# Performance work log

Hardware: AMD Instinct MI355X
Metric: run time of the kernel (lower is better)

Reference implementation:

```python
import jax, jax.numpy as jnp
import numpy as np

TOKENS, D_IN = 8192, 1024
E, D_OUT = 8, 1024
H = 2 * D_OUT  # Expert hidden = 2 * num_outputs


def setup_inputs() -> dict:
    key = jax.random.key(0)
    ks = jax.random.split(key, 4)
    s_in = 1.0 / np.sqrt(D_IN)
    s_h = 1.0 / np.sqrt(H)
    return {
        "x": jax.random.normal(ks[0], (TOKENS, D_IN), dtype=jnp.float32),
        "W1": jax.random.normal(ks[1], (E, D_IN, H), dtype=jnp.float32) * s_in,
        "b1": jnp.zeros((E, H), dtype=jnp.float32),
        "W2": jax.random.normal(ks[2], (E, H, D_OUT), dtype=jnp.float32) * s_h,
        "b2": jnp.zeros((E, D_OUT), dtype=jnp.float32),
        "Wg": jax.random.normal(ks[3], (D_IN, E), dtype=jnp.float32) * s_in,
        "bg": jnp.zeros((E,), dtype=jnp.float32),
    }


def reference(x, W1, b1, W2, b2, Wg, bg):
    # Gating: softmax over experts. gates: [N, E]
    gates = jax.nn.softmax(x @ Wg + bg, axis=-1)
    # All experts run densely: batched GEMM over expert axis.
    h = jax.nn.relu(jnp.einsum('nd,edh->neh', x, W1) + b1)       # [N, E, H]
    expert_out = jnp.einsum('neh,ehf->nef', h, W2) + b2          # [N, E, D_OUT]
    # Gate-weighted sum over experts (fused stack*gate->sum).
    return jnp.einsum('nef,ne->nf', expert_out, gates)            # [N, D_OUT]
```

## Files before the change

### kernel.cpp

```cpp
#include <hip/hip_runtime.h>
#include <stdint.h>

#define TOKENS 8192
#define D_IN   1024
#define NEXP   8
#define D_OUT  1024
#define HDIM   2048

typedef __bf16 bf16x8 __attribute__((ext_vector_type(8)));
typedef __bf16 bf16x4 __attribute__((ext_vector_type(4)));
typedef float  f32x4  __attribute__((ext_vector_type(4)));

__device__ __forceinline__ void gload16(const void* g, void* l) {
  __builtin_amdgcn_global_load_lds(
      (const __attribute__((address_space(1))) void*)g,
      (__attribute__((address_space(3))) void*)l,
      16, 0, 0);
}

template <int N>
__device__ __forceinline__ void waitv() {
  if constexpr (N == 0)      asm volatile("s_waitcnt vmcnt(0)" ::: "memory");
  else if constexpr (N == 1) asm volatile("s_waitcnt vmcnt(1)" ::: "memory");
  else if constexpr (N == 2) asm volatile("s_waitcnt vmcnt(2)" ::: "memory");
  else if constexpr (N == 3) asm volatile("s_waitcnt vmcnt(3)" ::: "memory");
  else if constexpr (N == 4) asm volatile("s_waitcnt vmcnt(4)" ::: "memory");
  else if constexpr (N == 5) asm volatile("s_waitcnt vmcnt(5)" ::: "memory");
  else if constexpr (N == 6) asm volatile("s_waitcnt vmcnt(6)" ::: "memory");
  else static_assert(N <= 6, "unsupported vmcnt");
}

__global__ void gate_cvt_kernel(const float* __restrict__ x,
                                const float* __restrict__ Wg,
                                const float* __restrict__ bg,
                                float* __restrict__ gates,
                                __bf16* __restrict__ xb) {
  const int lane = threadIdx.x & 63;
  const int n = blockIdx.x * 4 + (threadIdx.x >> 6);
  float acc[NEXP];
#pragma unroll
  for (int e = 0; e < NEXP; ++e) acc[e] = 0.f;
  const float* xr = x + (size_t)n * D_IN;
  __bf16* xo = xb + (size_t)n * D_IN;
#pragma unroll 4
  for (int d0 = 0; d0 < D_IN; d0 += 64) {
    const int d = d0 + lane;
    float xv = xr[d];
    xo[d] = (__bf16)xv;
    const float* wr = Wg + d * NEXP;
#pragma unroll
    for (int e = 0; e < NEXP; ++e) acc[e] += xv * wr[e];
  }
#pragma unroll
  for (int e = 0; e < NEXP; ++e) {
    float v = acc[e];
#pragma unroll
    for (int off = 32; off > 0; off >>= 1) v += __shfl_down(v, off);
    acc[e] = v;
  }
  if (lane == 0) {
    float mx = -1e30f;
#pragma unroll
    for (int e = 0; e < NEXP; ++e) { acc[e] += bg[e]; mx = fmaxf(mx, acc[e]); }
    float s = 0.f;
#pragma unroll
    for (int e = 0; e < NEXP; ++e) { acc[e] = expf(acc[e] - mx); s += acc[e]; }
    float inv = 1.f / s;
#pragma unroll
    for (int e = 0; e < NEXP; ++e) gates[n * NEXP + e] = acc[e] * inv;
  }
}

__global__ void transpose_cvt_kernel(const float* __restrict__ W,
                                     __bf16* __restrict__ Wt,
                                     int K, int N, int EPG) {
  __shared__ float tile[32][33];
  const int e = blockIdx.z;
  const int ldo = EPG * K;
  const float* Win = W + (size_t)e * K * N;
  __bf16* Wout = Wt + (size_t)(e / EPG) * N * ldo + (size_t)(e % EPG) * K;
  const int n0 = blockIdx.x * 32;
  const int k0 = blockIdx.y * 32;
  const int tx = threadIdx.x & 31;
  const int ty = threadIdx.x >> 5;
#pragma unroll
  for (int r = ty; r < 32; r += 8)
    tile[r][tx] = Win[(size_t)(k0 + r) * N + n0 + tx];
  __syncthreads();
#pragma unroll
  for (int r = ty; r < 32; r += 8)
    Wout[(size_t)(n0 + r) * ldo + k0 + tx] = (__bf16)tile[tx][r];
}

__global__ void merge_kernel(float* __restrict__ out,
                             const float* __restrict__ acc1,
                             const float* __restrict__ gates,
                             const float* __restrict__ b2,
                             int use_acc1) {
  const int idx = blockIdx.x * 256 + threadIdx.x;
  const int n = idx >> 8;
  const int fb = idx & 255;
  float4 o = ((const float4*)out)[idx];
  if (use_acc1) {
    float4 a = ((const float4*)acc1)[idx];
    o.x += a.x; o.y += a.y; o.z += a.z; o.w += a.w;
  }
  const float* g = gates + (size_t)n * NEXP;
#pragma unroll
  for (int e = 0; e < NEXP; ++e) {
    const float ge = g[e];
    float4 b = ((const float4*)(b2 + (size_t)e * D_OUT))[fb];
    o.x += ge * b.x; o.y += ge * b.y; o.z += ge * b.z; o.w += ge * b.w;
  }
  ((float4*)out)[idx] = o;
}

template <int NT, int BM, int BN, int WM, int WN, int EPI>
__global__ __launch_bounds__(NT, 2)
void moe_gemm(const __bf16* __restrict__ A, size_t AZ,
              const __bf16* __restrict__ B, size_t BZ,
              const float* __restrict__ b1g,
              const float* __restrict__ gates,
              int e0,
              __bf16* __restrict__ Hout, size_t HZ, int OCZ, int ldo,
              float* __restrict__ F0, float* __restrict__ F1,
              int first, int M, int N, int K) {
  constexpr int RM = BM / WM, RN = BN / WN;
  constexpr int FM = RM / 16, FN = RN / 16;
  constexpr int HM = FM / 2,  HN = FN / 2;
  constexpr int LA = BM * 4 / NT;
  constexpr int LB = BN * 4 / NT;
  constexpr int AELEM = BM * 64;
  static_assert(HM * HN * 2 == 16, "want 16-MFMA clusters");
  __shared__ alignas(16) __bf16 lds[(BM + BN) * 64];

  const int tid  = threadIdx.x;
  const int lane = tid & 63;
  const int wave = tid >> 6;
  const int wr   = wave / WN;
  const int wc   = wave % WN;
  const int lrow = lane & 15;
  const int khi  = lane >> 4;
  const int sx   = (lrow & 7) << 3;
  const int bz   = blockIdx.z;

  A += (size_t)bz * AZ;
  B += (size_t)bz * BZ;

  const int Gx   = gridDim.x;
  const int nwg  = Gx * gridDim.y;
  const int orig = blockIdx.y * Gx + blockIdx.x;
  const int wgid = (orig & 7) * (nwg >> 3) + (orig >> 3);
  const int bn0  = (wgid % Gx) * BN;
  const int bm0  = (wgid / Gx) * BM;

  const __bf16* srcA[2][LA];
  const __bf16* srcB[2][LB];
#pragma unroll
  for (int q = 0; q < 2; ++q) {
#pragma unroll
    for (int j = 0; j < LA; ++j) {
      int o   = q * (BM * 64) + j * (NT * 16) + tid * 16;
      int row = o >> 7;
      int cb  = (o & 127) ^ ((row & 7) << 4);
      srcA[q][j] = A + (size_t)(bm0 + row) * K + (cb >> 1);
    }
#pragma unroll
    for (int j = 0; j < LB; ++j) {
      int o   = q * (BN * 64) + j * (NT * 16) + tid * 16;
      int row = o >> 7;
      int cb  = (o & 127) ^ ((row & 7) << 4);
      srcB[q][j] = B + (size_t)(bn0 + row) * K + (cb >> 1);
    }
  }

  auto stageA = [&](int kt, int q) {
#pragma unroll
    for (int j = 0; j < LA; ++j)
      gload16(srcA[q][j] + (size_t)kt * 64,
              lds + q * (BM * 32) + j * (NT * 8) + wave * 512);
  };
  auto stageB = [&](int kt, int q) {
#pragma unroll
    for (int j = 0; j < LB; ++j)
      gload16(srcB[q][j] + (size_t)kt * 64,
              lds + AELEM + q * (BN * 32) + j * (NT * 8) + wave * 512);
  };

  f32x4 acc[FM][FN];
#pragma unroll
  for (int m = 0; m < FM; ++m)
#pragma unroll
    for (int n = 0; n < FN; ++n) acc[m][n] = f32x4{0.f, 0.f, 0.f, 0.f};

  bf16x8 af[HM][2];
  bf16x8 bf[2][HN][2];

  auto rdA = [&](int mq) {
#pragma unroll
    for (int mi = 0; mi < HM; ++mi)
#pragma unroll
      for (int kk = 0; kk < 2; ++kk)
        af[mi][kk] = *(const bf16x8*)
            &lds[(size_t)(mq * (BM / 2) + wr * (RM / 2) + mi * 16 + lrow) * 64 +
                 ((kk * 32 + khi * 8) ^ sx)];
  };
  auto rdB = [&](int nq) {
#pragma unroll
    for (int ni = 0; ni < HN; ++ni)
#pragma unroll
      for (int kk = 0; kk < 2; ++kk)
        bf[nq][ni][kk] = *(const bf16x8*)
            &lds[AELEM +
                 (size_t)(nq * (BN / 2) + wc * (RN / 2) + ni * 16 + lrow) * 64 +
                 ((kk * 32 + khi * 8) ^ sx)];
  };
  auto cluster = [&](int mq, int nq) {
    __builtin_amdgcn_s_setprio(1);
#pragma unroll
    for (int kk = 0; kk < 2; ++kk)
#pragma unroll
      for (int mi = 0; mi < HM; ++mi)
#pragma unroll
        for (int ni = 0; ni < HN; ++ni)
          acc[mq * HM + mi][nq * HN + ni] =
              __builtin_amdgcn_mfma_f32_16x16x32_bf16(
                  af[mi][kk], bf[nq][ni][kk], acc[mq * HM + mi][nq * HN + ni],
                  0, 0, 0);
    __builtin_amdgcn_s_setprio(0);
  };

#define BAR()   asm volatile("s_barrier" ::: "memory")
#define LGKM0() do { asm volatile("s_waitcnt lgkmcnt(0)" ::: "memory"); \
                     __builtin_amdgcn_sched_barrier(0); } while (0)

  const int nk = K >> 6;

  stageA(0, 0); stageB(0, 0); stageB(0, 1);
  waitv<LB>();
  BAR();

  for (int t = 0; t < nk; ++t) {
    const bool pf = (t + 1 < nk);

    rdA(0); rdB(0);
    stageA(t, 1);
    BAR(); LGKM0();
    cluster(0, 0);
    waitv<LA>();
    BAR();
    rdB(1);
    if (pf) stageA(t + 1, 0);
    BAR(); LGKM0();
    cluster(0, 1);
    if (pf) waitv<LA>(); else waitv<0>();
    BAR();
    rdA(1);
    if (pf) stageB(t + 1, 0);
    BAR(); LGKM0();
    cluster(1, 0);
    BAR();
    if (pf) stageB(t + 1, 1);
    BAR();
    cluster(1, 1);
    if (pf) waitv<LB>();
    BAR();
  }

#undef BAR
#undef LGKM0

  const float* bias = (EPI == 0) ? b1g + (size_t)(e0 + bz) * HDIM : nullptr;
  const int ecol = e0 + bz;
  __bf16* Hp = (EPI == 0) ? Hout + (size_t)bz * HZ + (size_t)bz * OCZ : nullptr;
  float* F = (EPI == 3) ? (bz ? F1 : F0) : nullptr;

#pragma unroll
  for (int m = 0; m < FM; ++m) {
    const int grow0 = bm0 + (m / HM) * (BM / 2) + wr * (RM / 2) +
                      (m % HM) * 16 + khi * 4;
    if constexpr (EPI == 0) {
      float g[4];
#pragma unroll
      for (int r = 0; r < 4; ++r)
        g[r] = gates[(size_t)(grow0 + r) * NEXP + ecol];
#pragma unroll
      for (int n = 0; n < FN; ++n) {
        const int gcol = bn0 + (n / HN) * (BN / 2) + wc * (RN / 2) +
                         (n % HN) * 16 + lrow;
        const float bv = bias[gcol];
        f32x4 a = acc[m][n];
#pragma unroll
        for (int r = 0; r < 4; ++r) {
          float v = a[r] + bv;
          v = v > 0.f ? v : 0.f;
          Hp[(size_t)(grow0 + r) * ldo + gcol] = (__bf16)(v * g[r]);
        }
      }
    } else {
#pragma unroll
      for (int n = 0; n < FN; ++n) {
        const int gcol = bn0 + (n / HN) * (BN / 2) + wc * (RN / 2) +
                         (n % HN) * 16 + lrow;
        f32x4 a = acc[m][n];
#pragma unroll
        for (int r = 0; r < 4; ++r) {
          float* o = F + (size_t)(grow0 + r) * N + gcol;
          if (first) *o = a[r];
          else       *o += a[r];
        }
      }
    }
  }
}

extern "C" void kernel_launch(void* const* d_in, const int* in_sizes, int n_in,
                              void* d_out, int out_size, void* d_ws, size_t ws_size,
                              hipStream_t stream) {
  const float* x  = (const float*)d_in[0];
  const float* W1 = (const float*)d_in[1];
  const float* b1 = (const float*)d_in[2];
  const float* W2 = (const float*)d_in[3];
  const float* b2 = (const float*)d_in[4];
  const float* Wg = (const float*)d_in[5];
  const float* bg = (const float*)d_in[6];
  float* out = (float*)d_out;

  char* w = (char*)d_ws;
  float* gates = (float*)w;   w += (size_t)TOKENS * NEXP * 4;
  __bf16* xb   = (__bf16*)w;  w += (size_t)TOKENS * D_IN * 2;
  __bf16* w1t  = (__bf16*)w;  w += (size_t)NEXP * HDIM * D_IN * 2;
  __bf16* w2c  = (__bf16*)w;  w += (size_t)NEXP * D_OUT * HDIM * 2;
  const size_t base = (size_t)(w - (char*)d_ws);

  const size_t acc_b = (size_t)TOKENS * D_OUT * 4;
  const size_t h1_b  = (size_t)TOKENS * HDIM * 2;
  const int G = (ws_size >= base + acc_b + 4 * h1_b) ? 4
              : (ws_size >= base + acc_b + 2 * h1_b) ? 2 : 1;

  float* acc1 = nullptr;
  if (G > 1) { acc1 = (float*)w; w += acc_b; }
  __bf16* hbuf = (__bf16*)w;

  const size_t WSLICE = (size_t)HDIM * D_IN;

  gate_cvt_kernel<<<TOKENS / 4, 256, 0, stream>>>(x, Wg, bg, gates, xb);
  transpose_cvt_kernel<<<dim3(HDIM / 32, D_IN / 32, NEXP), 256, 0, stream>>>(
      W1, w1t, D_IN, HDIM, 1);
  transpose_cvt_kernel<<<dim3(D_OUT / 32, HDIM / 32, NEXP), 256, 0, stream>>>(
      W2, w2c, HDIM, D_OUT, (G == 4) ? 2 : 1);

  if (G == 4) {
    for (int d = 0; d < 2; ++d) {
      for (int i2 = 0; i2 < 2; ++i2) {
        const int e0 = 4 * d + 2 * i2;
        moe_gemm<512, 256, 256, 2, 4, 0><<<dim3(8, 32, 2), 512, 0, stream>>>(
            xb, 0, w1t + (size_t)e0 * WSLICE, WSLICE, b1, gates, e0,
            hbuf + (size_t)i2 * TOKENS * 4096, 0, HDIM, 2 * HDIM,
            nullptr, nullptr, 0, TOKENS, HDIM, D_IN);
      }
      moe_gemm<256, 256, 128, 2, 2, 3><<<dim3(8, 32, 2), 256, 0, stream>>>(
          hbuf, (size_t)TOKENS * 4096,
          w2c + (size_t)(2 * d) * D_OUT * 4096, (size_t)D_OUT * 4096,
          nullptr, nullptr, 0, nullptr, 0, 0, 2 * HDIM,
          out, acc1, (d == 0) ? 1 : 0, TOKENS, D_OUT, 2 * HDIM);
    }
  } else if (G == 2) {
    for (int d = 0; d < 4; ++d) {
      const int e0 = 2 * d;
      moe_gemm<512, 256, 256, 2, 4, 0><<<dim3(8, 32, 2), 512, 0, stream>>>(
          xb, 0, w1t + (size_t)e0 * WSLICE, WSLICE, b1, gates, e0,
          hbuf, (size_t)TOKENS * HDIM, 0, HDIM,
          nullptr, nullptr, 0, TOKENS, HDIM, D_IN);
      moe_gemm<256, 256, 128, 2, 2, 3><<<dim3(8, 32, 2), 256, 0, stream>>>(
          hbuf, (size_t)TOKENS * HDIM,
          w2c + (size_t)e0 * D_OUT * HDIM, (size_t)D_OUT * HDIM,
          nullptr, nullptr, 0, nullptr, 0, 0, HDIM,
          out, acc1, (d == 0) ? 1 : 0, TOKENS, D_OUT, HDIM);
    }
  } else {
    for (int e = 0; e < NEXP; ++e) {
      moe_gemm<512, 256, 256, 2, 4, 0><<<dim3(8, 32, 1), 512, 0, stream>>>(
          xb, 0, w1t + (size_t)e * WSLICE, 0, b1, gates, e,
          hbuf, 0, 0, HDIM,
          nullptr, nullptr, 0, TOKENS, HDIM, D_IN);
      moe_gemm<256, 256, 128, 2, 2, 3><<<dim3(8, 32, 1), 256, 0, stream>>>(
          hbuf, 0, w2c + (size_t)e * D_OUT * HDIM, 0,
          nullptr, nullptr, 0, nullptr, 0, 0, HDIM,
          out, nullptr, (e == 0) ? 1 : 0, TOKENS, D_OUT, HDIM);
    }
  }

  merge_kernel<<<TOKENS, 256, 0, stream>>>(out, acc1, gates, b2, (G > 1) ? 1 : 0);
}
```

Measured before the change: 661.3 us.

## Split-K second GEMM with atomic accumulation into pre-initialized output

The second expert GEMM now uses the larger 512-thread 256x256 tile and splits its K dimension in two across grid z. Partial sums go straight into the output with float atomics instead of read-modify-write into two accumulators. A new init kernel writes the gate-weighted b2 bias into the output up front, which removes the acc1 buffer and the final merge pass. The cost is atomic traffic and result order that is no longer deterministic. The EPI value 4 must be handled by the epilogue code not shown here.

```diff
diff --git a/kernel.cpp b/kernel.cpp
--- a/kernel.cpp
+++ b/kernel.cpp
@@ -25,9 +25,7 @@
   else if constexpr (N == 2) asm volatile("s_waitcnt vmcnt(2)" ::: "memory");
   else if constexpr (N == 3) asm volatile("s_waitcnt vmcnt(3)" ::: "memory");
   else if constexpr (N == 4) asm volatile("s_waitcnt vmcnt(4)" ::: "memory");
-  else if constexpr (N == 5) asm volatile("s_waitcnt vmcnt(5)" ::: "memory");
-  else if constexpr (N == 6) asm volatile("s_waitcnt vmcnt(6)" ::: "memory");
-  else static_assert(N <= 6, "unsupported vmcnt");
+  else static_assert(N <= 4, "unsupported vmcnt");
 }
 
 __global__ void gate_cvt_kernel(const float* __restrict__ x,
@@ -92,19 +90,13 @@
     Wout[(size_t)(n0 + r) * ldo + k0 + tx] = (__bf16)tile[tx][r];
 }
 
-__global__ void merge_kernel(float* __restrict__ out,
-                             const float* __restrict__ acc1,
-                             const float* __restrict__ gates,
-                             const float* __restrict__ b2,
-                             int use_acc1) {
+__global__ void init_out_kernel(float* __restrict__ out,
+                                const float* __restrict__ gates,
+                                const float* __restrict__ b2) {
   const int idx = blockIdx.x * 256 + threadIdx.x;
   const int n = idx >> 8;
   const int fb = idx & 255;
-  float4 o = ((const float4*)out)[idx];
-  if (use_acc1) {
-    float4 a = ((const float4*)acc1)[idx];
-    o.x += a.x; o.y += a.y; o.z += a.z; o.w += a.w;
-  }
+  float4 o = {0.f, 0.f, 0.f, 0.f};
   const float* g = gates + (size_t)n * NEXP;
 #pragma unroll
   for (int e = 0; e < NEXP; ++e) {
@@ -119,12 +111,13 @@
 __global__ __launch_bounds__(NT, 2)
 void moe_gemm(const __bf16* __restrict__ A, size_t AZ,
               const __bf16* __restrict__ B, size_t BZ,
+              int NKH, int KHO,
               const float* __restrict__ b1g,
               const float* __restrict__ gates,
               int e0,
               __bf16* __restrict__ Hout, size_t HZ, int OCZ, int ldo,
-              float* __restrict__ F0, float* __restrict__ F1,
-              int first, int M, int N, int K) {
+              float* __restrict__ Fout,
+              int M, int N, int Kext, int LDK) {
   constexpr int RM = BM / WM, RN = BN / WN;
   constexpr int FM = RM / 16, FN = RN / 16;
   constexpr int HM = FM / 2,  HN = FN / 2;
@@ -143,9 +136,11 @@
   const int khi  = lane >> 4;
   const int sx   = (lrow & 7) << 3;
   const int bz   = blockIdx.z;
-
-  A += (size_t)bz * AZ;
-  B += (size_t)bz * BZ;
+  const int slice = bz / NKH;
+  const int kh    = bz % NKH;
+
+  A += (size_t)slice * AZ + (size_t)kh * KHO;
+  B += (size_t)slice * BZ + (size_t)kh * KHO;
 
   const int Gx   = gridDim.x;
   const int nwg  = Gx * gridDim.y;
@@ -163,14 +158,14 @@
       int o   = q * (BM * 64) + j * (NT * 16) + tid * 16;
       int row = o >> 7;
       int cb  = (o & 127) ^ ((row & 7) << 4);
-      srcA[q][j] = A + (size_t)(bm0 + row) * K + (cb >> 1);
+      srcA[q][j] = A + (size_t)(bm0 + row) * LDK + (cb >> 1);
     }
 #pragma unroll
     for (int j = 0; j < LB; ++j) {
       int o   = q * (BN * 64) + j * (NT * 16) + tid * 16;
       int row = o >> 7;
       int cb  = (o & 127) ^ ((row & 7) << 4);
-      srcB[q][j] = B + (size_t)(bn0 + row) * K + (cb >> 1);
+      srcB[q][j] = B + (size_t)(bn0 + row) * LDK + (cb >> 1);
     }
   }
 
@@ -234,7 +229,7 @@
 #define LGKM0() do { asm volatile("s_waitcnt lgkmcnt(0)" ::: "memory"); \
                      __builtin_amdgcn_sched_barrier(0); } while (0)
 
-  const int nk = K >> 6;
+  const int nk = Kext >> 6;
 
   stageA(0, 0); stageB(0, 0); stageB(0, 1);
   waitv<LB>();
@@ -270,10 +265,10 @@
 #undef BAR
 #undef LGKM0
 
-  const float* bias = (EPI == 0) ? b1g + (size_t)(e0 + bz) * HDIM : nullptr;
-  const int ecol = e0 + bz;
-  __bf16* Hp = (EPI == 0) ? Hout + (size_t)bz * HZ + (size_t)bz * OCZ : nullptr;
-  float* F = (EPI == 3) ? (bz ? F1 : F0) : nullptr;
+  const float* bias = (EPI == 0) ? b1g + (size_t)(e0 + slice) * HDIM : nullptr;
+  const int ecol = e0 + slice;
+  __bf16* Hp = (EPI == 0) ? Hout + (size_t)slice * HZ + (size_t)slice * OCZ
+                          : nullptr;
 
 #pragma unroll
   for (int m = 0; m < FM; ++m) {
@@ -304,11 +299,8 @@
                          (n % HN) * 16 + lrow;
         f32x4 a = acc[m][n];
 #pragma unroll
-        for (int r = 0; r < 4; ++r) {
-          float* o = F + (size_t)(grow0 + r) * N + gcol;
-          if (first) *o = a[r];
-          else       *o += a[r];
-        }
+        for (int r = 0; r < 4; ++r)
+          unsafeAtomicAdd(Fout + (size_t)(grow0 + r) * N + gcol, a[r]);
       }
     }
   }
@@ -333,18 +325,15 @@
   __bf16* w2c  = (__bf16*)w;  w += (size_t)NEXP * D_OUT * HDIM * 2;
   const size_t base = (size_t)(w - (char*)d_ws);
 
-  const size_t acc_b = (size_t)TOKENS * D_OUT * 4;
-  const size_t h1_b  = (size_t)TOKENS * HDIM * 2;
-  const int G = (ws_size >= base + acc_b + 4 * h1_b) ? 4
-              : (ws_size >= base + acc_b + 2 * h1_b) ? 2 : 1;
-
-  float* acc1 = nullptr;
-  if (G > 1) { acc1 = (float*)w; w += acc_b; }
+  const size_t h1_b = (size_t)TOKENS * HDIM * 2;
+  const int G = (ws_size >= base + 4 * h1_b) ? 4
+              : (ws_size >= base + 2 * h1_b) ? 2 : 1;
   __bf16* hbuf = (__bf16*)w;
 
   const size_t WSLICE = (size_t)HDIM * D_IN;
 
   gate_cvt_kernel<<<TOKENS / 4, 256, 0, stream>>>(x, Wg, bg, gates, xb);
+  init_out_kernel<<<TOKENS, 256, 0, stream>>>(out, gates, b2);
   transpose_cvt_kernel<<<dim3(HDIM / 32, D_IN / 32, NEXP), 256, 0, stream>>>(
       W1, w1t, D_IN, HDIM, 1);
   transpose_cvt_kernel<<<dim3(D_OUT / 32, HDIM / 32, NEXP), 256, 0, stream>>>(
@@ -355,41 +344,39 @@
       for (int i2 = 0; i2 < 2; ++i2) {
         const int e0 = 4 * d + 2 * i2;
         moe_gemm<512, 256, 256, 2, 4, 0><<<dim3(8, 32, 2), 512, 0, stream>>>(
-            xb, 0, w1t + (size_t)e0 * WSLICE, WSLICE, b1, gates, e0,
+            xb, 0, w1t + (size_t)e0 * WSLICE, WSLICE, 1, 0, b1, gates, e0,
             hbuf + (size_t)i2 * TOKENS * 4096, 0, HDIM, 2 * HDIM,
-            nullptr, nullptr, 0, TOKENS, HDIM, D_IN);
+            nullptr, TOKENS, HDIM, D_IN, D_IN);
       }
-      moe_gemm<256, 256, 128, 2, 2, 3><<<dim3(8, 32, 2), 256, 0, stream>>>(
+      moe_gemm<512, 256, 256, 2, 4, 4><<<dim3(4, 32, 4), 512, 0, stream>>>(
           hbuf, (size_t)TOKENS * 4096,
           w2c + (size_t)(2 * d) * D_OUT * 4096, (size_t)D_OUT * 4096,
-          nullptr, nullptr, 0, nullptr, 0, 0, 2 * HDIM,
-          out, acc1, (d == 0) ? 1 : 0, TOKENS, D_OUT, 2 * HDIM);
+          2, 2048, nullptr, nullptr, 0, nullptr, 0, 0, 0,
+          out, TOKENS, D_OUT, 2048, 4096);
     }
   } else if (G == 2) {
     for (int d = 0; d < 4; ++d) {
       const int e0 = 2 * d;
       moe_gemm<512, 256, 256, 2, 4, 0><<<dim3(8, 32, 2), 512, 0, stream>>>(
-          xb, 0, w1t + (size_t)e0 * WSLICE, WSLICE, b1, gates, e0,
+          xb, 0, w1t + (size_t)e0 * WSLICE, WSLICE, 1, 0, b1, gates, e0,
           hbuf, (size_t)TOKENS * HDIM, 0, HDIM,
-          nullptr, nullptr, 0, TOKENS, HDIM, D_IN);
-      moe_gemm<256, 256, 128, 2, 2, 3><<<dim3(8, 32, 2), 256, 0, stream>>>(
+          nullptr, TOKENS, HDIM, D_IN, D_IN);
+      moe_gemm<512, 256, 256, 2, 4, 4><<<dim3(4, 32, 4), 512, 0, stream>>>(
           hbuf, (size_t)TOKENS * HDIM,
           w2c + (size_t)e0 * D_OUT * HDIM, (size_t)D_OUT * HDIM,
-          nullptr, nullptr, 0, nullptr, 0, 0, HDIM,
-          out, acc1, (d == 0) ? 1 : 0, TOKENS, D_OUT, HDIM);
+          2, 1024, nullptr, nullptr, 0, nullptr, 0, 0, 0,
+          out, TOKENS, D_OUT, 1024, HDIM);
     }
   } else {
     for (int e = 0; e < NEXP; ++e) {
       moe_gemm<512, 256, 256, 2, 4, 0><<<dim3(8, 32, 1), 512, 0, stream>>>(
-          xb, 0, w1t + (size_t)e * WSLICE, 0, b1, gates, e,
+          xb, 0, w1t + (size_t)e * WSLICE, 0, 1, 0, b1, gates, e,
           hbuf, 0, 0, HDIM,
-          nullptr, nullptr, 0, TOKENS, HDIM, D_IN);
-      moe_gemm<256, 256, 128, 2, 2, 3><<<dim3(8, 32, 1), 256, 0, stream>>>(
+          nullptr, TOKENS, HDIM, D_IN, D_IN);
+      moe_gemm<512, 256, 256, 2, 4, 4><<<dim3(4, 32, 2), 512, 0, stream>>>(
           hbuf, 0, w2c + (size_t)e * D_OUT * HDIM, 0,
-          nullptr, nullptr, 0, nullptr, 0, 0, HDIM,
-          out, nullptr, (e == 0) ? 1 : 0, TOKENS, D_OUT, HDIM);
-    }
-  }
-
-  merge_kernel<<<TOKENS, 256, 0, stream>>>(out, acc1, gates, b2, (G > 1) ? 1 : 0);
-}
+          2, 1024, nullptr, nullptr, 0, nullptr, 0, 0, 0,
+          out, TOKENS, D_OUT, 1024, HDIM);
+    }
+  }
+}
```

Measured after the change: 766.9 us. 1.16x slower.

## Double-buffer LDS in second expert GEMM and widen its tile to 256x256

Applied to the files above, without the earlier changes.

Adds a DBUF template parameter so the second (down-projection) GEMM keeps two LDS stages, prefetching the whole next K-tile into the alternate slot while the current one is consumed. That GEMM also moves from a 256x128 tile with 256 threads to a 256x256 tile with 512 threads, halving the grid's x dimension. The aim is to hide global-load latency and raise operand reuse per block. The cost is 128 KB of LDS per block, which limits occupancy to one block per CU and may conflict with the launch_bounds hint of two blocks.

```diff
diff --git a/kernel.cpp b/kernel.cpp
--- a/kernel.cpp
+++ b/kernel.cpp
@@ -115,7 +115,7 @@
   ((float4*)out)[idx] = o;
 }
 
-template <int NT, int BM, int BN, int WM, int WN, int EPI>
+template <int NT, int BM, int BN, int WM, int WN, int EPI, int DBUF>
 __global__ __launch_bounds__(NT, 2)
 void moe_gemm(const __bf16* __restrict__ A, size_t AZ,
               const __bf16* __restrict__ B, size_t BZ,
@@ -131,8 +131,9 @@
   constexpr int LA = BM * 4 / NT;
   constexpr int LB = BN * 4 / NT;
   constexpr int AELEM = BM * 64;
+  constexpr int SLOT  = (BM + BN) * 64;
   static_assert(HM * HN * 2 == 16, "want 16-MFMA clusters");
-  __shared__ alignas(16) __bf16 lds[(BM + BN) * 64];
+  __shared__ alignas(16) __bf16 lds[DBUF * SLOT];
 
   const int tid  = threadIdx.x;
   const int lane = tid & 63;
@@ -174,17 +175,17 @@
     }
   }
 
-  auto stageA = [&](int kt, int q) {
+  auto stageA = [&](int kt, int q, int s) {
 #pragma unroll
     for (int j = 0; j < LA; ++j)
       gload16(srcA[q][j] + (size_t)kt * 64,
-              lds + q * (BM * 32) + j * (NT * 8) + wave * 512);
+              lds + s * SLOT + q * (BM * 32) + j * (NT * 8) + wave * 512);
   };
-  auto stageB = [&](int kt, int q) {
+  auto stageB = [&](int kt, int q, int s) {
 #pragma unroll
     for (int j = 0; j < LB; ++j)
       gload16(srcB[q][j] + (size_t)kt * 64,
-              lds + AELEM + q * (BN * 32) + j * (NT * 8) + wave * 512);
+              lds + s * SLOT + AELEM + q * (BN * 32) + j * (NT * 8) + wave * 512);
   };
 
   f32x4 acc[FM][FN];
@@ -196,24 +197,23 @@
   bf16x8 af[HM][2];
   bf16x8 bf[2][HN][2];
 
-  auto rdA = [&](int mq) {
+  auto rdA = [&](const __bf16* As, int mq) {
 #pragma unroll
     for (int mi = 0; mi < HM; ++mi)
 #pragma unroll
       for (int kk = 0; kk < 2; ++kk)
         af[mi][kk] = *(const bf16x8*)
-            &lds[(size_t)(mq * (BM / 2) + wr * (RM / 2) + mi * 16 + lrow) * 64 +
-                 ((kk * 32 + khi * 8) ^ sx)];
+            &As[(size_t)(mq * (BM / 2) + wr * (RM / 2) + mi * 16 + lrow) * 64 +
+                ((kk * 32 + khi * 8) ^ sx)];
   };
-  auto rdB = [&](int nq) {
+  auto rdB = [&](const __bf16* Bs, int nq) {
 #pragma unroll
     for (int ni = 0; ni < HN; ++ni)
 #pragma unroll
       for (int kk = 0; kk < 2; ++kk)
         bf[nq][ni][kk] = *(const bf16x8*)
-            &lds[AELEM +
-                 (size_t)(nq * (BN / 2) + wc * (RN / 2) + ni * 16 + lrow) * 64 +
-                 ((kk * 32 + khi * 8) ^ sx)];
+            &Bs[(size_t)(nq * (BN / 2) + wc * (RN / 2) + ni * 16 + lrow) * 64 +
+                ((kk * 32 + khi * 8) ^ sx)];
   };
   auto cluster = [&](int mq, int nq) {
     __builtin_amdgcn_s_setprio(1);
@@ -236,35 +236,67 @@
 
   const int nk = K >> 6;
 
-  stageA(0, 0); stageB(0, 0); stageB(0, 1);
-  waitv<LB>();
-  BAR();
-
-  for (int t = 0; t < nk; ++t) {
-    const bool pf = (t + 1 < nk);
-
-    rdA(0); rdB(0);
-    stageA(t, 1);
-    BAR(); LGKM0();
-    cluster(0, 0);
-    waitv<LA>();
+  if constexpr (DBUF == 1) {
+    stageA(0, 0, 0); stageB(0, 0, 0); stageB(0, 1, 0);
+    waitv<LB>();
     BAR();
-    rdB(1);
-    if (pf) stageA(t + 1, 0);
-    BAR(); LGKM0();
-    cluster(0, 1);
-    if (pf) waitv<LA>(); else waitv<0>();
+    for (int t = 0; t < nk; ++t) {
+      const bool pf = (t + 1 < nk);
+      rdA(lds, 0); rdB(lds + AELEM, 0);
+      stageA(t, 1, 0);
+      BAR(); LGKM0();
+      cluster(0, 0);
+      waitv<LA>();
+      BAR();
+      rdB(lds + AELEM, 1);
+      if (pf) stageA(t + 1, 0, 0);
+      BAR(); LGKM0();
+      cluster(0, 1);
+      if (pf) waitv<LA>(); else waitv<0>();
+      BAR();
+      rdA(lds, 1);
+      if (pf) stageB(t + 1, 0, 0);
+      BAR(); LGKM0();
+      cluster(1, 0);
+      BAR();
+      if (pf) stageB(t + 1, 1, 0);
+      BAR();
+      cluster(1, 1);
+      if (pf) waitv<LB>();
+      BAR();
+    }
+  } else {
+    stageA(0, 0, 0); stageB(0, 0, 0); stageB(0, 1, 0); stageA(0, 1, 0);
+    waitv<LA + LB>();
     BAR();
-    rdA(1);
-    if (pf) stageB(t + 1, 0);
-    BAR(); LGKM0();
-    cluster(1, 0);
-    BAR();
-    if (pf) stageB(t + 1, 1);
-    BAR();
-    cluster(1, 1);
-    if (pf) waitv<LB>();
-    BAR();
+    for (int t = 0; t < nk; ++t) {
+      const int s = t & 1;
+      const __bf16* As = lds + s * SLOT;
+      const __bf16* Bs = As + AELEM;
+      const bool pf = (t + 1 < nk);
+      rdA(As, 0); rdB(Bs, 0);
+      if (pf) stageA(t + 1, 0, s ^ 1);
+      BAR(); LGKM0();
+      cluster(0, 0);
+      if (pf) waitv<2 * LA>(); else waitv<LA>();
+      BAR();
+      rdB(Bs, 1);
+      if (pf) stageB(t + 1, 0, s ^ 1);
+      BAR(); LGKM0();
+      cluster(0, 1);
+      if (pf) waitv<LA + LB>(); else waitv<0>();
+      BAR();
+      rdA(As, 1);
+      if (pf) stageB(t + 1, 1, s ^ 1);
+      BAR(); LGKM0();
+      cluster(1, 0);
+      BAR();
+      if (pf) stageA(t + 1, 1, s ^ 1);
+      BAR();
+      cluster(1, 1);
+      if (pf) waitv<LA + LB>();
+      BAR();
+    }
   }
 
 #undef BAR
@@ -354,39 +386,39 @@
     for (int d = 0; d < 2; ++d) {
       for (int i2 = 0; i2 < 2; ++i2) {
         const int e0 = 4 * d + 2 * i2;
-        moe_gemm<512, 256, 256, 2, 4, 0><<<dim3(8, 32, 2), 512, 0, stream>>>(
+        moe_gemm<512, 256, 256, 2, 4, 0, 1><<<dim3(8, 32, 2), 512, 0, stream>>>(
             xb, 0, w1t + (size_t)e0 * WSLICE, WSLICE, b1, gates, e0,
             hbuf + (size_t)i2 * TOKENS * 4096, 0, HDIM, 2 * HDIM,
             nullptr, nullptr, 0, TOKENS, HDIM, D_IN);
       }
-      moe_gemm<256, 256, 128, 2, 2, 3><<<dim3(8, 32, 2), 256, 0, stream>>>(
+      moe_gemm<512, 256, 256, 2, 4, 3, 2><<<dim3(4, 32, 2), 512, 0, stream>>>(
           hbuf, (size_t)TOKENS * 4096,
           w2c + (size_t)(2 * d) * D_OUT * 4096, (size_t)D_OUT * 4096,
-          nullptr, nullptr, 0, nullptr, 0, 0, 2 * HDIM,
+          nullptr, nullptr, 0, nullptr, 0, 0, 0,
           out, acc1, (d == 0) ? 1 : 0, TOKENS, D_OUT, 2 * HDIM);
     }
   } else if (G == 2) {
     for (int d = 0; d < 4; ++d) {
       const int e0 = 2 * d;
-      moe_gemm<512, 256, 256, 2, 4, 0><<<dim3(8, 32, 2), 512, 0, stream>>>(
+      moe_gemm<512, 256, 256, 2, 4, 0, 1><<<dim3(8, 32, 2), 512, 0, stream>>>(
           xb, 0, w1t + (size_t)e0 * WSLICE, WSLICE, b1, gates, e0,
           hbuf, (size_t)TOKENS * HDIM, 0, HDIM,
           nullptr, nullptr, 0, TOKENS, HDIM, D_IN);
-      moe_gemm<256, 256, 128, 2, 2, 3><<<dim3(8, 32, 2), 256, 0, stream>>>(
+      moe_gemm<512, 256, 256, 2, 4, 3, 2><<<dim3(4, 32, 2), 512, 0, stream>>>(
           hbuf, (size_t)TOKENS * HDIM,
           w2c + (size_t)e0 * D_OUT * HDIM, (size_t)D_OUT * HDIM,
-          nullptr, nullptr, 0, nullptr, 0, 0, HDIM,
+          nullptr, nullptr, 0, nullptr, 0, 0, 0,
           out, acc1, (d == 0) ? 1 : 0, TOKENS, D_OUT, HDIM);
     }
   } else {
     for (int e = 0; e < NEXP; ++e) {
-      moe_gemm<512, 256, 256, 2, 4, 0><<<dim3(8, 32, 1), 512, 0, stream>>>(
+      moe_gemm<512, 256, 256, 2, 4, 0, 1><<<dim3(8, 32, 1), 512, 0, stream>>>(
           xb, 0, w1t + (size_t)e * WSLICE, 0, b1, gates, e,
           hbuf, 0, 0, HDIM,
           nullptr, nullptr, 0, TOKENS, HDIM, D_IN);
-      moe_gemm<256, 256, 128, 2, 2, 3><<<dim3(8, 32, 1), 256, 0, stream>>>(
+      moe_gemm<512, 256, 256, 2, 4, 3, 2><<<dim3(4, 32, 1), 512, 0, stream>>>(
           hbuf, 0, w2c + (size_t)e * D_OUT * HDIM, 0,
-          nullptr, nullptr, 0, nullptr, 0, 0, HDIM,
+          nullptr, nullptr, 0, nullptr, 0, 0, 0,
           out, nullptr, (e == 0) ? 1 : 0, TOKENS, D_OUT, HDIM);
     }
   }
```

New measurement: 659.2 us. No clear change (-0.3%).

## Concatenate expert hidden states along K and run single-output second GEMM

Applied to the files above, without the earlier changes.

The first GEMM now writes each expert's hidden activations side by side in one wide row buffer (stride G*HDIM), so the second GEMM becomes a single long-K GEMM per group instead of a batched split into two partial outputs. This drops the separate acc1 accumulator, its workspace and the extra read in the merge kernel, and reduces read-modify-write passes over the output. The second GEMM switches to 128x128 tiles with a higher occupancy hint (3 blocks per CU), which gives more blocks but less reuse per tile.

```diff
diff --git a/kernel.cpp b/kernel.cpp
--- a/kernel.cpp
+++ b/kernel.cpp
@@ -25,9 +25,7 @@
   else if constexpr (N == 2) asm volatile("s_waitcnt vmcnt(2)" ::: "memory");
   else if constexpr (N == 3) asm volatile("s_waitcnt vmcnt(3)" ::: "memory");
   else if constexpr (N == 4) asm volatile("s_waitcnt vmcnt(4)" ::: "memory");
-  else if constexpr (N == 5) asm volatile("s_waitcnt vmcnt(5)" ::: "memory");
-  else if constexpr (N == 6) asm volatile("s_waitcnt vmcnt(6)" ::: "memory");
-  else static_assert(N <= 6, "unsupported vmcnt");
+  else static_assert(N <= 4, "unsupported vmcnt");
 }
 
 __global__ void gate_cvt_kernel(const float* __restrict__ x,
@@ -93,18 +91,12 @@
 }
 
 __global__ void merge_kernel(float* __restrict__ out,
-                             const float* __restrict__ acc1,
                              const float* __restrict__ gates,
-                             const float* __restrict__ b2,
-                             int use_acc1) {
+                             const float* __restrict__ b2) {
   const int idx = blockIdx.x * 256 + threadIdx.x;
   const int n = idx >> 8;
   const int fb = idx & 255;
   float4 o = ((const float4*)out)[idx];
-  if (use_acc1) {
-    float4 a = ((const float4*)acc1)[idx];
-    o.x += a.x; o.y += a.y; o.z += a.z; o.w += a.w;
-  }
   const float* g = gates + (size_t)n * NEXP;
 #pragma unroll
   for (int e = 0; e < NEXP; ++e) {
@@ -115,15 +107,15 @@
   ((float4*)out)[idx] = o;
 }
 
-template <int NT, int BM, int BN, int WM, int WN, int EPI>
-__global__ __launch_bounds__(NT, 2)
+template <int NT, int WPE, int BM, int BN, int WM, int WN, int EPI>
+__global__ __launch_bounds__(NT, WPE)
 void moe_gemm(const __bf16* __restrict__ A, size_t AZ,
               const __bf16* __restrict__ B, size_t BZ,
               const float* __restrict__ b1g,
               const float* __restrict__ gates,
               int e0,
-              __bf16* __restrict__ Hout, size_t HZ, int OCZ, int ldo,
-              float* __restrict__ F0, float* __restrict__ F1,
+              __bf16* __restrict__ Hout, int OCZ, int ldo,
+              float* __restrict__ F0,
               int first, int M, int N, int K) {
   constexpr int RM = BM / WM, RN = BN / WN;
   constexpr int FM = RM / 16, FN = RN / 16;
@@ -131,7 +123,7 @@
   constexpr int LA = BM * 4 / NT;
   constexpr int LB = BN * 4 / NT;
   constexpr int AELEM = BM * 64;
-  static_assert(HM * HN * 2 == 16, "want 16-MFMA clusters");
+  static_assert(HM >= 1 && HN >= 1, "tile too small");
   __shared__ alignas(16) __bf16 lds[(BM + BN) * 64];
 
   const int tid  = threadIdx.x;
@@ -272,8 +264,7 @@
 
   const float* bias = (EPI == 0) ? b1g + (size_t)(e0 + bz) * HDIM : nullptr;
   const int ecol = e0 + bz;
-  __bf16* Hp = (EPI == 0) ? Hout + (size_t)bz * HZ + (size_t)bz * OCZ : nullptr;
-  float* F = (EPI == 3) ? (bz ? F1 : F0) : nullptr;
+  __bf16* Hp = (EPI == 0) ? Hout + (size_t)bz * OCZ : nullptr;
 
 #pragma unroll
   for (int m = 0; m < FM; ++m) {
@@ -305,7 +296,7 @@
         f32x4 a = acc[m][n];
 #pragma unroll
         for (int r = 0; r < 4; ++r) {
-          float* o = F + (size_t)(grow0 + r) * N + gcol;
+          float* o = F0 + (size_t)(grow0 + r) * N + gcol;
           if (first) *o = a[r];
           else       *o += a[r];
         }
@@ -333,63 +324,42 @@
   __bf16* w2c  = (__bf16*)w;  w += (size_t)NEXP * D_OUT * HDIM * 2;
   const size_t base = (size_t)(w - (char*)d_ws);
 
-  const size_t acc_b = (size_t)TOKENS * D_OUT * 4;
-  const size_t h1_b  = (size_t)TOKENS * HDIM * 2;
-  const int G = (ws_size >= base + acc_b + 4 * h1_b) ? 4
-              : (ws_size >= base + acc_b + 2 * h1_b) ? 2 : 1;
-
-  float* acc1 = nullptr;
-  if (G > 1) { acc1 = (float*)w; w += acc_b; }
+  const size_t h1_b = (size_t)TOKENS * HDIM * 2;
+  const int G = (ws_size >= base + 4 * h1_b) ? 4
+              : (ws_size >= base + 2 * h1_b) ? 2 : 1;
   __bf16* hbuf = (__bf16*)w;
 
   const size_t WSLICE = (size_t)HDIM * D_IN;
+  const int KB = G * HDIM;
 
   gate_cvt_kernel<<<TOKENS / 4, 256, 0, stream>>>(x, Wg, bg, gates, xb);
   transpose_cvt_kernel<<<dim3(HDIM / 32, D_IN / 32, NEXP), 256, 0, stream>>>(
       W1, w1t, D_IN, HDIM, 1);
   transpose_cvt_kernel<<<dim3(D_OUT / 32, HDIM / 32, NEXP), 256, 0, stream>>>(
-      W2, w2c, HDIM, D_OUT, (G == 4) ? 2 : 1);
-
-  if (G == 4) {
-    for (int d = 0; d < 2; ++d) {
-      for (int i2 = 0; i2 < 2; ++i2) {
-        const int e0 = 4 * d + 2 * i2;
-        moe_gemm<512, 256, 256, 2, 4, 0><<<dim3(8, 32, 2), 512, 0, stream>>>(
+      W2, w2c, HDIM, D_OUT, G);
+
+  const int ngroups = NEXP / G;
+  for (int d = 0; d < ngroups; ++d) {
+    if (G >= 2) {
+      for (int i2 = 0; i2 < G / 2; ++i2) {
+        const int e0 = G * d + 2 * i2;
+        moe_gemm<512, 2, 256, 256, 2, 4, 0><<<dim3(8, 32, 2), 512, 0, stream>>>(
             xb, 0, w1t + (size_t)e0 * WSLICE, WSLICE, b1, gates, e0,
-            hbuf + (size_t)i2 * TOKENS * 4096, 0, HDIM, 2 * HDIM,
-            nullptr, nullptr, 0, TOKENS, HDIM, D_IN);
+            hbuf + (size_t)i2 * 2 * HDIM, HDIM, KB,
+            nullptr, 0, TOKENS, HDIM, D_IN);
       }
-      moe_gemm<256, 256, 128, 2, 2, 3><<<dim3(8, 32, 2), 256, 0, stream>>>(
-          hbuf, (size_t)TOKENS * 4096,
-          w2c + (size_t)(2 * d) * D_OUT * 4096, (size_t)D_OUT * 4096,
-          nullptr, nullptr, 0, nullptr, 0, 0, 2 * HDIM,
-          out, acc1, (d == 0) ? 1 : 0, TOKENS, D_OUT, 2 * HDIM);
+    } else {
+      moe_gemm<512, 2, 256, 256, 2, 4, 0><<<dim3(8, 32, 1), 512, 0, stream>>>(
+          xb, 0, w1t + (size_t)d * WSLICE, 0, b1, gates, d,
+          hbuf, 0, KB,
+          nullptr, 0, TOKENS, HDIM, D_IN);
     }
-  } else if (G == 2) {
-    for (int d = 0; d < 4; ++d) {
-      const int e0 = 2 * d;
-      moe_gemm<512, 256, 256, 2, 4, 0><<<dim3(8, 32, 2), 512, 0, stream>>>(
-          xb, 0, w1t + (size_t)e0 * WSLICE, WSLICE, b1, gates, e0,
-          hbuf, (size_t)TOKENS * HDIM, 0, HDIM,
-          nullptr, nullptr, 0, TOKENS, HDIM, D_IN);
-      moe_gemm<256, 256, 128, 2, 2, 3><<<dim3(8, 32, 2), 256, 0, stream>>>(
-          hbuf, (size_t)TOKENS * HDIM,
-          w2c + (size_t)e0 * D_OUT * HDIM, (size_t)D_OUT * HDIM,
-          nullptr, nullptr, 0, nullptr, 0, 0, HDIM,
-          out, acc1, (d == 0) ? 1 : 0, TOKENS, D_OUT, HDIM);
-    }
-  } else {
-    for (int e = 0; e < NEXP; ++e) {
-      moe_gemm<512, 256, 256, 2, 4, 0><<<dim3(8, 32, 1), 512, 0, stream>>>(
-          xb, 0, w1t + (size_t)e * WSLICE, 0, b1, gates, e,
-          hbuf, 0, 0, HDIM,
-          nullptr, nullptr, 0, TOKENS, HDIM, D_IN);
-      moe_gemm<256, 256, 128, 2, 2, 3><<<dim3(8, 32, 1), 256, 0, stream>>>(
-          hbuf, 0, w2c + (size_t)e * D_OUT * HDIM, 0,
-          nullptr, nullptr, 0, nullptr, 0, 0, HDIM,
-          out, nullptr, (e == 0) ? 1 : 0, TOKENS, D_OUT, HDIM);
-    }
-  }
-
-  merge_kernel<<<TOKENS, 256, 0, stream>>>(out, acc1, gates, b2, (G > 1) ? 1 : 0);
-}
+    moe_gemm<256, 3, 128, 128, 2, 2, 3><<<dim3(D_OUT / 128, TOKENS / 128, 1),
+                                          256, 0, stream>>>(
+        hbuf, 0, w2c + (size_t)d * D_OUT * KB, 0,
+        nullptr, nullptr, 0, nullptr, 0, 0,
+        out, (d == 0) ? 1 : 0, TOKENS, D_OUT, KB);
+  }
+
+  merge_kernel<<<TOKENS, 256, 0, stream>>>(out, gates, b2);
+}
```

Result: faster. 645.5 us (-2.4%).
